# Performance work log

Hardware: AMD Instinct MI355X
Metric: run time of the kernel (lower is better)

Reference implementation:

```python
import jax, jax.numpy as jnp
import numpy as np

BS, L, D = 16, 256, 512
H, DQ, DV, DFF, KSZ = 8, 64, 64, 2048, 3


def _ln(x, g, b, eps=1e-5):
    mu = jnp.mean(x, -1, keepdims=True)
    var = jnp.mean((x - mu) ** 2, -1, keepdims=True)
    return (x - mu) / jnp.sqrt(var + eps) * g + b


def _conv(x, w):
    # x: [bs, 1, d] (NCW), w: [1, 1, k], same padding for odd k, no bias
    pad = (w.shape[-1] - 1) // 2
    return jax.lax.conv_general_dilated(x, w, (1,), [(pad, pad)], dimension_numbers=('NCH', 'OIH', 'NCH'))


def setup_inputs() -> dict:
    key = jax.random.key(0)
    ks = jax.random.split(key, 12)
    s = lambda k, shape, sc: jax.random.normal(k, shape, jnp.float32) * sc
    w0 = 0.02
    return {
        'inp': jax.random.normal(ks[0], (BS, L, D), jnp.float32),
        'conv1_w': s(ks[1], (1, 1, KSZ), 0.3),
        'conv2_w': s(ks[2], (1, 1, KSZ), 0.3),
        'ctx_wq': s(ks[3], (D, H * DQ), w0),
        'ctx_wk': s(ks[4], (D, H * DQ), w0),
        'ctx_fc': s(ks[5], (H * DV, D), w0),
        'glb_wq': s(ks[6], (D, H * DQ), w0),
        'glb_wk': s(ks[7], (D, H * DQ), w0),
        'glb_fc': s(ks[8], (H * DV, D), w0),
        'ln1_g': jnp.ones(D), 'ln1_b': jnp.zeros(D),
        'ln2_g': jnp.ones(D), 'ln2_b': jnp.zeros(D),
        'ln3_g': jnp.ones(D), 'ln3_b': jnp.zeros(D),
        'mlp_w1': s(ks[9], (D, DFF), w0), 'mlp_b1': jnp.zeros(DFF),
        'mlp_w2': s(ks[10], (DFF, D), w0), 'mlp_b2': jnp.zeros(D),
    }


def reference(inp, conv1_w, conv2_w, ctx_wq, ctx_wk, ctx_fc,
              glb_wq, glb_wk, glb_fc, ln1_g, ln1_b, ln2_g, ln2_b,
              ln3_g, ln3_b, mlp_w1, mlp_b1, mlp_w2, mlp_b2):
    bs, seqlen, d = inp.shape
    scale = 1.0 / jnp.sqrt(jnp.float32(DQ))
    # Global K/V are step-invariant: hoist out of the recurrence.
    # NOTE: original module (faithfully) projects V with W_Q, not W_V.
    Kg = (inp @ glb_wk).reshape(bs, seqlen, H, DQ).transpose(0, 2, 1, 3)  # [b,h,L,dq]
    Vg = (inp @ glb_wq).reshape(bs, seqlen, H, DV).transpose(0, 2, 1, 3)  # [b,h,L,dv]

    def step(hn, x_i):
        # hn: [bs,1,d] recurrent state, x_i: [bs,d] current token
        x = x_i[:, None, :]                                   # [bs,1,d]
        res = x
        xc = _conv(x, conv1_w)                                # [bs,1,d]
        # context cross-attn: Q=hn, K=xc, V=xc (via W_Q, as in source)
        Qc = (hn @ ctx_wq).reshape(bs, 1, H, DQ).transpose(0, 2, 1, 3)
        Kc = (xc @ ctx_wk).reshape(bs, 1, H, DQ).transpose(0, 2, 1, 3)
        Vc = (xc @ ctx_wq).reshape(bs, 1, H, DV).transpose(0, 2, 1, 3)
        sc = jnp.einsum('bhqd,bhkd->bhqk', Qc, Kc) * scale    # [b,h,1,1]
        ac = jax.nn.softmax(sc, axis=-1)
        ctx = jnp.einsum('bhqk,bhkd->bhqd', ac, Vc)
        ctx = ctx.transpose(0, 2, 1, 3).reshape(bs, 1, H * DV) @ ctx_fc
        x = _ln(ctx + res, ln1_g, ln1_b)
        res = x
        x2 = _conv(x, conv2_w)
        # global cross-attn: Q=x2, K/V from full input (hoisted)
        Qg = (x2 @ glb_wq).reshape(bs, 1, H, DQ).transpose(0, 2, 1, 3)
        sg = jnp.einsum('bhqd,bhkd->bhqk', Qg, Kg) * scale    # [b,h,1,L]
        h = jnp.einsum('bhqk,bhkd->bhqd', jax.nn.softmax(sg, axis=-1), Vg)
        h = h.transpose(0, 2, 1, 3).reshape(bs, 1, H * DV) @ glb_fc  # [bs,1,d]
        x = _ln(h + res, ln2_g, ln2_b)
        y = jax.nn.gelu(x @ mlp_w1 + mlp_b1, approximate=False) @ mlp_w2 + mlp_b2
        y = _ln(y + x, ln3_g, ln3_b)
        return h, y[:, 0, :]

    hn0 = inp[:, 0:1, :]
    hn, ys = jax.lax.scan(step, hn0, jnp.swapaxes(inp, 0, 1))  # ys: [L,bs,d]
    output = jnp.swapaxes(ys, 0, 1)                            # [bs,L,d]
    return output, hn
```

## Files before the change

kernel.cpp:

```cpp
#include <hip/hip_runtime.h>
#include <math.h>

#define NBS 16
#define NL 256
#define ND 512
#define NH 8
#define NDFF 2048
#define NT (NBS*NL)

typedef unsigned short u16;
typedef unsigned int   u32;
typedef __attribute__((ext_vector_type(8))) short bf16x8;
typedef __attribute__((ext_vector_type(4))) float f32x4;

__device__ __forceinline__ u16 f2b(float f){
  u32 u = __float_as_uint(f);
  u32 r = u + 0x7FFFu + ((u >> 16) & 1u);
  return (u16)(r >> 16);
}
__device__ __forceinline__ float blo(u32 u){ return __uint_as_float(u << 16); }
__device__ __forceinline__ float bhi(u32 u){ return __uint_as_float(u & 0xFFFF0000u); }
__device__ __forceinline__ u32 pk2(float a, float b){ return (u32)f2b(a) | ((u32)f2b(b) << 16); }

__device__ __forceinline__ void gl16(const void* g, void* l){
  __builtin_amdgcn_global_load_lds((const __attribute__((address_space(1))) void*)g,
                                   (__attribute__((address_space(3))) void*)l, 16, 0, 0);
}
__device__ __forceinline__ float gelu_f(float x){ return 0.5f*x*(1.f+erff(x*0.70710678118654752f)); }

__device__ inline void tr_tile(const float* __restrict__ src, u16* __restrict__ dst,
                               int K, int N, int ntk, int tb, float* Tsh){
  int tk = tb % ntk, tn = tb / ntk;
  int t = threadIdx.x;
  int r = t >> 2, q = t & 3;
  const float* s = src + (size_t)(tk*64 + r)*N + tn*64 + q*16;
  #pragma unroll
  for (int u2 = 0; u2 < 4; u2++){
    float4 v = *(const float4*)(s + u2*4);
    Tsh[r*65 + q*16 + u2*4 + 0] = v.x;
    Tsh[r*65 + q*16 + u2*4 + 1] = v.y;
    Tsh[r*65 + q*16 + u2*4 + 2] = v.z;
    Tsh[r*65 + q*16 + u2*4 + 3] = v.w;
  }
  __syncthreads();
  int n = t >> 2, kq = t & 3;
  u16* d = dst + (size_t)(tn*64 + n)*K + tk*64 + kq*16;
  u32 u[8];
  #pragma unroll
  for (int j = 0; j < 8; j++){
    u32 lo = f2b(Tsh[(kq*16 + 2*j    )*65 + n]);
    u32 hi = f2b(Tsh[(kq*16 + 2*j + 1)*65 + n]);
    u[j] = lo | (hi << 16);
  }
  ((uint4*)d)[0] = make_uint4(u[0],u[1],u[2],u[3]);
  ((uint4*)d)[1] = make_uint4(u[4],u[5],u[6],u[7]);
}

__global__ __launch_bounds__(256) void pack_k(
    const float* __restrict__ inp,
    const float* __restrict__ ctx_wq, const float* __restrict__ ctx_fc,
    const float* __restrict__ glb_wq, const float* __restrict__ glb_wk,
    const float* __restrict__ glb_fc,
    const float* __restrict__ w1, const float* __restrict__ w2,
    const float* __restrict__ c1w,
    u16* wk_t, u16* wq_t, u16* cfc_t, u16* gfc_t, u16* cwq_bf,
    u16* w1_t, u16* w2_t, u16* inp_bf, u16* xc_bf)
{
  __shared__ float Tsh[64*65];
  int bx = blockIdx.x, t = threadIdx.x;
  if (bx < 256){
    int m = bx >> 6, tb = bx & 63;
    const float* s; u16* d;
    if      (m == 0){ s = glb_wk; d = wk_t; }
    else if (m == 1){ s = glb_wq; d = wq_t; }
    else if (m == 2){ s = ctx_fc; d = cfc_t; }
    else            { s = glb_fc; d = gfc_t; }
    tr_tile(s, d, 512, 512, 8, tb, Tsh);
  } else if (bx < 512){
    tr_tile(w1, w1_t, 512, 2048, 8, bx - 256, Tsh);
  } else if (bx < 768){
    tr_tile(w2, w2_t, 2048, 512, 32, bx - 512, Tsh);
  } else if (bx < 1792){
    size_t i0 = (size_t)(bx - 768)*2048 + (size_t)t*8;
    float4 v0 = *(const float4*)(inp + i0);
    float4 v1 = *(const float4*)(inp + i0 + 4);
    uint4 o;
    o.x = pk2(v0.x, v0.y); o.y = pk2(v0.z, v0.w);
    o.z = pk2(v1.x, v1.y); o.w = pk2(v1.z, v1.w);
    *(uint4*)(inp_bf + i0) = o;
  } else if (bx < 2816){
    size_t i0 = (size_t)(bx - 1792)*2048 + (size_t)t*8;
    float w0 = c1w[0], w1v = c1w[1], w2v = c1w[2];
    u32 u[4];
    #pragma unroll
    for (int j = 0; j < 8; j += 2){
      float f[2];
      #pragma unroll
      for (int s2 = 0; s2 < 2; s2++){
        size_t i = i0 + j + s2; int d = (int)(i & (ND-1));
        float xm = d        ? inp[i-1] : 0.f;
        float x0 = inp[i];
        float xp = (d<ND-1) ? inp[i+1] : 0.f;
        f[s2] = w0*xm + w1v*x0 + w2v*xp;
      }
      u[j>>1] = pk2(f[0], f[1]);
    }
    *(uint4*)(xc_bf + i0) = make_uint4(u[0],u[1],u[2],u[3]);
  } else {
    size_t i0 = (size_t)(bx - 2816)*2048 + (size_t)t*8;
    float4 v0 = *(const float4*)(ctx_wq + i0);
    float4 v1 = *(const float4*)(ctx_wq + i0 + 4);
    uint4 o;
    o.x = pk2(v0.x, v0.y); o.y = pk2(v0.z, v0.w);
    o.z = pk2(v1.x, v1.y); o.w = pk2(v1.z, v1.w);
    *(uint4*)(cwq_bf + i0) = o;
  }
}

template<int BIAS,int ACT>
__device__ __forceinline__ void gemm128_core(const u16* __restrict__ A,
    const u16* __restrict__ Bt, const float* __restrict__ bias,
    void* __restrict__ Cb, int N, int K, int lda, int ldb, int outm,
    u16* sm, int row0, int col0)
{
  const int tid = threadIdx.x;
  const int w = tid >> 6, l = tid & 63;
  const int wr = w >> 1, wc = w & 1;
  const int l15 = l & 15, lk = (l >> 4)*16;
  const int srow = tid >> 3;
  const int scol = (((tid & 7)*16) ^ ((srow & 7) << 4)) >> 1;
  const u16* pa = A  + (size_t)(row0 + srow)*lda + scol;
  const u16* pb = Bt + (size_t)(col0 + srow)*ldb + scol;
  char* lA = (char*)sm + (tid & ~63)*16;
  char* lB = (char*)sm + 32768 + (tid & ~63)*16;

  f32x4 acc[4][4] = {};
  const int nt = K >> 6;

  auto STAGE = [&](int buf, int kt){
    char* a = lA + buf*16384;
    char* b = lB + buf*16384;
    #pragma unroll
    for (int i = 0; i < 4; i++){
      gl16(pa + kt + (size_t)(i*32)*lda, a + i*4096);
      gl16(pb + kt + (size_t)(i*32)*ldb, b + i*4096);
    }
  };

  STAGE(0, 0);
  __syncthreads();
  for (int t = 0; t < nt; ++t){
    if (t + 1 < nt) STAGE((t+1) & 1, (t+1)*64);
    const char* bA = (const char*)sm + (t&1)*16384;
    const char* bB = (const char*)sm + 32768 + (t&1)*16384;
    #pragma unroll
    for (int ks = 0; ks < 2; ks++){
      bf16x8 af[4], bv[4];
      #pragma unroll
      for (int m = 0; m < 4; m++){
        int r = wr*64 + m*16 + l15;
        af[m] = *(const bf16x8*)(bA + r*128 + ((ks*64 + lk) ^ ((r & 7) << 4)));
      }
      #pragma unroll
      for (int n = 0; n < 4; n++){
        int r = wc*64 + n*16 + l15;
        bv[n] = *(const bf16x8*)(bB + r*128 + ((ks*64 + lk) ^ ((r & 7) << 4)));
      }
      #pragma unroll
      for (int m = 0; m < 4; m++)
        #pragma unroll
        for (int n = 0; n < 4; n++)
          acc[m][n] = __builtin_amdgcn_mfma_f32_16x16x32_bf16(af[m], bv[n], acc[m][n], 0, 0, 0);
    }
    __syncthreads();
  }

  #pragma unroll
  for (int m = 0; m < 4; m++){
    #pragma unroll
    for (int n = 0; n < 4; n++){
      int col = col0 + wc*64 + n*16 + l15;
      int rowb = row0 + wr*64 + m*16 + (l >> 4)*4;
      if (outm == 2){
        uint2 o;
        o.x = pk2(acc[m][n][0], acc[m][n][1]);
        o.y = pk2(acc[m][n][2], acc[m][n][3]);
        *(uint2*)((u16*)Cb + (size_t)(rowb >> 8)*131072 + (size_t)col*256 + (rowb & 255)) = o;
      } else if (outm == 0){
        #pragma unroll
        for (int rr = 0; rr < 4; rr++)
          ((float*)Cb)[(size_t)(rowb + rr)*N + col] = acc[m][n][rr];
      } else {
        #pragma unroll
        for (int rr = 0; rr < 4; rr++){
          float v = acc[m][n][rr];
          if (BIAS) v += bias[col];
          if (ACT)  v = gelu_f(v);
          ((u16*)Cb)[(size_t)(rowb + rr)*N + col] = f2b(v);
        }
      }
    }
  }
}

template<int BIAS,int ACT>
__global__ __launch_bounds__(256) void gemm128_k(const u16* __restrict__ A,
                                                 const u16* __restrict__ Bt,
                                                 const float* __restrict__ bias,
                                                 void* __restrict__ Cb, int N, int K)
{
  __shared__ u16 sm[32768];
  gemm128_core<BIAS,ACT>(A, Bt, bias, Cb, N, K, K, K, 1, sm,
                         blockIdx.y*128, blockIdx.x*128);
}

__global__ __launch_bounds__(256) void gemm3_k(
    const u16* __restrict__ A0, const u16* __restrict__ B0, u16* __restrict__ C0,
    const u16* __restrict__ A1, const u16* __restrict__ B1, u16* __restrict__ C1,
    const u16* __restrict__ A2, const u16* __restrict__ B2, u16* __restrict__ C2)
{
  __shared__ u16 sm[32768];
  const u16 *A, *Bt; u16* Cb; int outm = 1;
  if (blockIdx.z == 0){ A = A0; Bt = B0; Cb = C0; }
  else if (blockIdx.z == 1){ A = A1; Bt = B1; Cb = C1; outm = 2; }
  else { A = A2; Bt = B2; Cb = C2; }
  gemm128_core<0,0>(A, Bt, nullptr, Cb, 512, 512, 512, 512, outm, sm,
                    blockIdx.y*128, blockIdx.x*128);
}

__global__ __launch_bounds__(256) void gemm_w2sk(const u16* __restrict__ G,
                                                 const u16* __restrict__ w2t,
                                                 float* __restrict__ P)
{
  __shared__ u16 sm[32768];
  const int z = blockIdx.z;
  gemm128_core<0,0>(G + z*1024, w2t + z*1024, nullptr,
                    (void*)(P + (size_t)z*NT*512), 512, 1024, 2048, 2048, 0,
                    sm, blockIdx.y*128, blockIdx.x*128);
}

__global__ __launch_bounds__(256) void gemm64_k(const u16* __restrict__ A,
                                                const u16* __restrict__ Bt,
                                                u16* __restrict__ Cb, int N, int K)
{
  __shared__ u16 sm[16384];
  const int tid = threadIdx.x;
  const int w = tid >> 6, l = tid & 63;
  const int wr = w >> 1, wc = w & 1;
  const int l15 = l & 15, lk = (l >> 4)*16;
  const int row0 = blockIdx.y*64, col0 = blockIdx.x*64;
  const int srow = tid >> 3;
  const int scol = (((tid & 7)*16) ^ ((srow & 7) << 4)) >> 1;
  const u16* pa = A  + (size_t)(row0 + srow)*K + scol;
  const u16* pb = Bt + (size_t)(col0 + srow)*K + scol;
  char* lA = (char*)sm + (tid & ~63)*16;

  f32x4 acc[2][2] = {};
  const int nt = K >> 6;
  auto STAGE = [&](int buf, int kt){
    char* a = lA + buf*8192;
    char* b = lA + 16384 + buf*8192;
    gl16(pa + kt,                a);
    gl16(pa + kt + (size_t)32*K, a + 4096);
    gl16(pb + kt,                b);
    gl16(pb + kt + (size_t)32*K, b + 4096);
  };
  STAGE(0, 0);
  __syncthreads();
  for (int t = 0; t < nt; ++t){
    if (t + 1 < nt) STAGE((t+1) & 1, (t+1)*64);
    const char* bA = (const char*)sm + (t&1)*8192;
    const char* bB = (const char*)sm + 16384 + (t&1)*8192;
    #pragma unroll
    for (int ks = 0; ks < 2; ks++){
      bf16x8 af[2], bv[2];
      #pragma unroll
      for (int m = 0; m < 2; m++){
        int r = wr*32 + m*16 + l15;
        af[m] = *(const bf16x8*)(bA + r*128 + ((ks*64 + lk) ^ ((r & 7) << 4)));
      }
      #pragma unroll
      for (int n = 0; n < 2; n++){
        int r = wc*32 + n*16 + l15;
        bv[n] = *(const bf16x8*)(bB + r*128 + ((ks*64 + lk) ^ ((r & 7) << 4)));
      }
      #pragma unroll
      for (int m = 0; m < 2; m++)
        #pragma unroll
        for (int n = 0; n < 2; n++)
          acc[m][n] = __builtin_amdgcn_mfma_f32_16x16x32_bf16(af[m], bv[n], acc[m][n], 0, 0, 0);
    }
    __syncthreads();
  }
  #pragma unroll
  for (int m = 0; m < 2; m++){
    #pragma unroll
    for (int n = 0; n < 2; n++){
      int col = col0 + wc*32 + n*16 + l15;
      int rowb = row0 + wr*32 + m*16 + (l >> 4)*4;
      #pragma unroll
      for (int rr = 0; rr < 4; rr++)
        Cb[(size_t)(rowb + rr)*N + col] = f2b(acc[m][n][rr]);
    }
  }
}

__global__ __launch_bounds__(256) void qattn_k(const u16* __restrict__ X2,
                                               const u16* __restrict__ Wq,
                                               const u16* __restrict__ Kg,
                                               const u16* __restrict__ Vt,
                                               u16* __restrict__ O)
{
  __shared__ u16 sm[40960];
  const int h = blockIdx.x, ty = blockIdx.y;
  const int b = ty >> 2, bh = b*8 + h;
  const int tid = threadIdx.x;
  const int w = tid >> 6, l = tid & 63;
  const int l15 = l & 15, lg = l >> 4;
  const int wr = w >> 1, wc = w & 1;
  const int lk = lg*16;

  {
    const int vrow = tid >> 5;
    const int vcb  = (tid*16) & 511;
    const int scolV = (vcb ^ ((vrow & 7) << 4)) >> 1;
    const u16* pv = Vt + (size_t)bh*16384 + (size_t)vrow*256 + scolV;
    char* lV = (char*)sm + 40960 + (tid & ~63)*16;
    #pragma unroll
    for (int c = 0; c < 8; c++)
      gl16(pv + (size_t)(c*8)*256, lV + c*4096);
  }

  const int srow = tid >> 3;
  const int scol = (((tid & 7)*16) ^ ((srow & 7) << 4)) >> 1;
  const u16* pa = X2 + (size_t)(ty*64 + srow)*512 + scol;
  const u16* pb = Wq + (size_t)(h*64  + srow)*512 + scol;
  char* lS = (char*)sm + (tid & ~63)*16;

  auto QSTG = [&](int buf, int kt){
    char* a = lS + buf*8192;
    char* bq = lS + 16384 + buf*8192;
    gl16(pa + kt,              a);
    gl16(pa + kt + 32*512,     a + 4096);
    gl16(pb + kt,              bq);
    gl16(pb + kt + 32*512,     bq + 4096);
  };

  f32x4 qacc[2][2] = {};
  QSTG(0, 0);
  __syncthreads();
  for (int t = 0; t < 8; ++t){
    if (t < 7) QSTG((t+1) & 1, (t+1)*64);
    const char* bA = (const char*)sm + (t&1)*8192;
    const char* bB = (const char*)sm + 16384 + (t&1)*8192;
    #pragma unroll
    for (int ks = 0; ks < 2; ks++){
      bf16x8 af[2], bv[2];
      #pragma unroll
      for (int m = 0; m < 2; m++){
        int r = wr*32 + m*16 + l15;
        af[m] = *(const bf16x8*)(bA + r*128 + ((ks*64 + lk) ^ ((r & 7) << 4)));
      }
      #pragma unroll
      for (int n = 0; n < 2; n++){
        int r = wc*32 + n*16 + l15;
        bv[n] = *(const bf16x8*)(bB + r*128 + ((ks*64 + lk) ^ ((r & 7) << 4)));
      }
      #pragma unroll
      for (int m = 0; m < 2; m++)
        #pragma unroll
        for (int n = 0; n < 2; n++)
          qacc[m][n] = __builtin_amdgcn_mfma_f32_16x16x32_bf16(af[m], bv[n], qacc[m][n], 0, 0, 0);
    }
    __syncthreads();
  }

  {
    const u16* pk = Kg + (size_t)(b*256 + srow)*512 + h*64 + scol;
    char* lK = (char*)sm + (tid & ~63)*16;
    #pragma unroll
    for (int c = 0; c < 8; c++)
      gl16(pk + (size_t)(c*32)*512, lK + c*4096);
  }
  #pragma unroll
  for (int m = 0; m < 2; m++)
    #pragma unroll
    for (int n = 0; n < 2; n++)
      #pragma unroll
      for (int rr = 0; rr < 4; rr++){
        int row = wr*32 + m*16 + (l >> 4)*4 + rr;
        int col = wc*32 + n*16 + l15;
        *(u16*)((char*)sm + 32768 + row*128 + ((col*2) ^ ((row & 7) << 4))) = f2b(qacc[m][n][rr]);
      }
  __syncthreads();

  const int qt0 = b*256 + (ty & 3)*64 + w*16;
  bf16x8 aq[2];
  #pragma unroll
  for (int ks = 0; ks < 2; ks++){
    int qr = w*16 + l15;
    aq[ks] = *(const bf16x8*)((char*)sm + 32768 + qr*128 + ((ks*64 + lk) ^ ((qr & 7) << 4)));
  }
  char* Pw = (char*)sm + 73728 + w*2048;

  f32x4 oacc[4] = {};
  float rsum[4] = {0.f, 0.f, 0.f, 0.f};

  #pragma unroll
  for (int c = 0; c < 4; c++){
    f32x4 sacc[4] = {};
    #pragma unroll
    for (int n = 0; n < 4; n++){
      int r = c*64 + n*16 + l15;
      #pragma unroll
      for (int ks = 0; ks < 2; ks++){
        bf16x8 bk = *(const bf16x8*)((const char*)sm + r*128 + ((ks*64 + lk) ^ ((r & 7) << 4)));
        sacc[n] = __builtin_amdgcn_mfma_f32_16x16x32_bf16(aq[ks], bk, sacc[n], 0, 0, 0);
      }
    }
    #pragma unroll
    for (int n = 0; n < 4; n++){
      #pragma unroll
      for (int rr = 0; rr < 4; rr++){
        float p = __expf(sacc[n][rr]*0.125f);
        rsum[rr] += p;
        int q = lg*4 + rr, key = n*16 + l15;
        *(u16*)(Pw + ((q*128 + key*2) ^ ((q & 7) << 4))) = f2b(p);
      }
    }
    bf16x8 ap[2];
    #pragma unroll
    for (int ks2 = 0; ks2 < 2; ks2++)
      ap[ks2] = *(const bf16x8*)(Pw + l15*128 + ((ks2*64 + lk) ^ ((l15 & 7) << 4)));
    #pragma unroll
    for (int n = 0; n < 4; n++){
      int r = n*16 + l15;
      #pragma unroll
      for (int ks2 = 0; ks2 < 2; ks2++){
        bf16x8 bvv = *(const bf16x8*)((const char*)sm + 40960 + r*512 +
                                      ((c*128 + ks2*64 + lk) ^ ((r & 7) << 4)));
        oacc[n] = __builtin_amdgcn_mfma_f32_16x16x32_bf16(ap[ks2], bvv, oacc[n], 0, 0, 0);
      }
    }
  }

  #pragma unroll
  for (int m = 1; m < 16; m <<= 1){
    #pragma unroll
    for (int rr = 0; rr < 4; rr++) rsum[rr] += __shfl_xor(rsum[rr], m);
  }
  #pragma unroll
  for (int n = 0; n < 4; n++){
    int d = h*64 + n*16 + l15;
    #pragma unroll
    for (int rr = 0; rr < 4; rr++){
      int t = qt0 + lg*4 + rr;
      O[(size_t)t*ND + d] = f2b(oacc[n][rr]/rsum[rr]);
    }
  }
}

template<int MODE>
__global__ __launch_bounds__(256) void ln_k(const void* __restrict__ aptr,
                                            const void* __restrict__ bptr,
                                            const float* __restrict__ g,
                                            const float* __restrict__ be,
                                            const float* __restrict__ cw,
                                            const float* __restrict__ a2,
                                            const float* __restrict__ bias2,
                                            u16* __restrict__ obf,
                                            u16* __restrict__ convbf,
                                            float* __restrict__ of32,
                                            float* __restrict__ hnout)
{
  __shared__ float row[512];
  __shared__ float red[10];
  const int r0 = blockIdx.x, tid = threadIdx.x;
  const size_t base = (size_t)r0*ND;
  const int d = tid*2;
  float v0, v1;
  if (MODE == 3){
    float2 p0 = *(const float2*)((const float*)aptr + base + d);
    float2 p1 = *(const float2*)(a2 + base + d);
    u32 bv = *(const u32*)((const u16*)bptr + base + d);
    v0 = p0.x + p1.x + bias2[d]   + blo(bv);
    v1 = p0.y + p1.y + bias2[d+1] + bhi(bv);
  } else {
    u32 av = *(const u32*)((const u16*)aptr + base + d);
    v0 = blo(av); v1 = bhi(av);
    if (MODE == 1 && (r0 & 255) == 255){
      hnout[(size_t)(r0 >> 8)*512 + d]     = v0;
      hnout[(size_t)(r0 >> 8)*512 + d + 1] = v1;
    }
    if (MODE == 0){
      float2 bv = *(const float2*)((const float*)bptr + base + d);
      v0 += bv.x; v1 += bv.y;
    } else {
      u32 bv = *(const u32*)((const u16*)bptr + base + d);
      v0 += blo(bv); v1 += bhi(bv);
    }
  }
  float s = v0+v1, ss = v0*v0+v1*v1;
  #pragma unroll
  for (int m = 1; m < 64; m <<= 1){ s += __shfl_xor(s, m); ss += __shfl_xor(ss, m); }
  int wv = tid >> 6;
  if ((tid & 63) == 0){ red[wv] = s; red[4+wv] = ss; }
  __syncthreads();
  if (tid == 0){
    float S = red[0]+red[1]+red[2]+red[3];
    float SS = red[4]+red[5]+red[6]+red[7];
    float mu = S*(1.f/ND);
    float var = SS*(1.f/ND) - mu*mu;
    red[8] = mu; red[9] = rsqrtf(var + 1e-5f);
  }
  __syncthreads();
  float mu = red[8], rsd = red[9];
  float o0 = (v0-mu)*rsd*g[d]   + be[d];
  float o1 = (v1-mu)*rsd*g[d+1] + be[d+1];
  if (MODE == 3){
    *(float2*)(of32 + base + d) = make_float2(o0, o1);
  } else {
    *(u32*)(obf + base + d) = pk2(o0, o1);
    if (MODE == 0){
      row[d] = o0; row[d+1] = o1;
      __syncthreads();
      float w0 = cw[0], w1v = cw[1], w2v = cw[2];
      float xm = d ? row[d-1] : 0.f;
      float xp2 = (d+2 < 512) ? row[d+2] : 0.f;
      float c0 = w0*xm + w1v*o0 + w2v*o1;
      float c1 = w0*o0 + w1v*o1 + w2v*xp2;
      *(u32*)(convbf + base + d) = pk2(c0, c1);
    }
  }
}

extern "C" void kernel_launch(void* const* d_in, const int* in_sizes, int n_in,
                              void* d_out, int out_size, void* d_ws, size_t ws_size,
                              hipStream_t stream) {
  const float* inp     = (const float*)d_in[0];
  const float* conv1_w = (const float*)d_in[1];
  const float* conv2_w = (const float*)d_in[2];
  const float* ctx_wq  = (const float*)d_in[3];
  const float* ctx_fc  = (const float*)d_in[5];
  const float* glb_wq  = (const float*)d_in[6];
  const float* glb_wk  = (const float*)d_in[7];
  const float* glb_fc  = (const float*)d_in[8];
  const float* ln1_g = (const float*)d_in[9],  *ln1_b = (const float*)d_in[10];
  const float* ln2_g = (const float*)d_in[11], *ln2_b = (const float*)d_in[12];
  const float* ln3_g = (const float*)d_in[13], *ln3_b = (const float*)d_in[14];
  const float* mlp_w1 = (const float*)d_in[15], *mlp_b1 = (const float*)d_in[16];
  const float* mlp_w2 = (const float*)d_in[17], *mlp_b2 = (const float*)d_in[18];
  float* out = (float*)d_out;
  float* hn  = out + (size_t)NT*ND;

  u16* wk_t   = (u16*)d_ws;
  u16* wq_t   = wk_t   + 262144;
  u16* cfc_t  = wq_t   + 262144;
  u16* gfc_t  = cfc_t  + 262144;
  u16* cwq_bf = gfc_t  + 262144;
  u16* Wc_t   = cwq_bf + 262144;
  u16* w1_t   = Wc_t   + 262144;
  u16* w2_t   = w1_t   + 1048576;
  u16* inp_bf = w2_t   + 1048576;
  u16* Abf    = inp_bf + 2097152;
  u16* Bbf    = Abf    + 2097152;
  u16* Cbf    = Bbf    + 2097152;
  u16* Kg     = Cbf    + 2097152;
  u16* Vt     = Kg     + 2097152;
  u16* X1bf   = Vt     + 2097152;
  u16* X3bf   = X1bf   + 2097152;
  u16* Gbf    = X3bf   + 2097152;
  float* Pf   = (float*)(Gbf + 8388608);

  pack_k<<<2944, 256, 0, stream>>>(inp, ctx_wq, ctx_fc, glb_wq, glb_wk, glb_fc,
                                   mlp_w1, mlp_w2, conv1_w,
                                   wk_t, wq_t, cfc_t, gfc_t, cwq_bf, w1_t, w2_t,
                                   inp_bf, Abf);
  gemm64_k<<<dim3(8,8),256,0,stream>>>(cfc_t, cwq_bf, Wc_t, 512, 512);
  gemm3_k<<<dim3(4,32,3),256,0,stream>>>(inp_bf, wk_t, Kg,
                                         inp_bf, wq_t, Vt,
                                         Abf,    Wc_t, Cbf);
  ln_k<0><<<NT,256,0,stream>>>(Cbf, inp, ln1_g, ln1_b, conv2_w, nullptr, nullptr,
                               X1bf, Abf, nullptr, nullptr);
  qattn_k<<<dim3(8,64),256,0,stream>>>(Abf, wq_t, Kg, Vt, Bbf);
  gemm64_k<<<dim3(8,64),256,0,stream>>>(Bbf, gfc_t, Cbf, 512, 512);
  ln_k<1><<<NT,256,0,stream>>>(Cbf, X1bf, ln2_g, ln2_b, nullptr, nullptr, nullptr,
                               X3bf, nullptr, nullptr, hn);
  gemm128_k<1,1><<<dim3(16,32),256,0,stream>>>(X3bf, w1_t, mlp_b1, Gbf, 2048, 512);
  gemm_w2sk<<<dim3(4,32,2),256,0,stream>>>(Gbf, w2_t, Pf);
  ln_k<3><<<NT,256,0,stream>>>(Pf, X3bf, ln3_g, ln3_b, nullptr, Pf + (size_t)NT*512,
                               mlp_b2, nullptr, nullptr, out, nullptr);
}
```

Baseline: 104.3 us.

## Shrink GEMM tiles and drop LDS double-buffering for higher occupancy

Replaces the 128x128 double-buffered GEMM core and the separate 64x64 kernel with one templated core using TMx64 tiles (TM=64 or 128) and a single LDS buffer, synchronised before and after each K-tile load. Launch grids are enlarged to match: more blocks for the QKV, MLP-up and MLP-down GEMMs, and smaller LDS and register footprints per block. The aim is more blocks and waves per CU on these mid-sized GEMMs. The cost is losing the load/compute overlap from double buffering and getting less data reuse per tile.

```diff
diff --git a/kernel.cpp b/kernel.cpp
--- a/kernel.cpp
+++ b/kernel.cpp
@@ -117,12 +117,13 @@
   }
 }
 
-template<int BIAS,int ACT>
-__device__ __forceinline__ void gemm128_core(const u16* __restrict__ A,
+template<int TM,int BIAS,int ACT>
+__device__ __forceinline__ void gemm2p_core(const u16* __restrict__ A,
     const u16* __restrict__ Bt, const float* __restrict__ bias,
     void* __restrict__ Cb, int N, int K, int lda, int ldb, int outm,
     u16* sm, int row0, int col0)
 {
+  constexpr int MF = TM/32;
   const int tid = threadIdx.x;
   const int w = tid >> 6, l = tid & 63;
   const int wr = w >> 1, wc = w & 1;
@@ -132,55 +133,48 @@
   const u16* pa = A  + (size_t)(row0 + srow)*lda + scol;
   const u16* pb = Bt + (size_t)(col0 + srow)*ldb + scol;
   char* lA = (char*)sm + (tid & ~63)*16;
-  char* lB = (char*)sm + 32768 + (tid & ~63)*16;
-
-  f32x4 acc[4][4] = {};
+  char* lB = (char*)sm + TM*128 + (tid & ~63)*16;
+
+  f32x4 acc[MF][2] = {};
   const int nt = K >> 6;
 
-  auto STAGE = [&](int buf, int kt){
-    char* a = lA + buf*16384;
-    char* b = lB + buf*16384;
-    #pragma unroll
-    for (int i = 0; i < 4; i++){
-      gl16(pa + kt + (size_t)(i*32)*lda, a + i*4096);
-      gl16(pb + kt + (size_t)(i*32)*ldb, b + i*4096);
-    }
-  };
-
-  STAGE(0, 0);
-  __syncthreads();
   for (int t = 0; t < nt; ++t){
-    if (t + 1 < nt) STAGE((t+1) & 1, (t+1)*64);
-    const char* bA = (const char*)sm + (t&1)*16384;
-    const char* bB = (const char*)sm + 32768 + (t&1)*16384;
+    __syncthreads();
+    #pragma unroll
+    for (int i = 0; i < MF; i++)
+      gl16(pa + t*64 + (size_t)(i*32)*lda, lA + i*4096);
+    gl16(pb + t*64,                  lB);
+    gl16(pb + t*64 + (size_t)32*ldb, lB + 4096);
+    __syncthreads();
+    const char* bA = (const char*)sm;
+    const char* bB = (const char*)sm + TM*128;
     #pragma unroll
     for (int ks = 0; ks < 2; ks++){
-      bf16x8 af[4], bv[4];
-      #pragma unroll
-      for (int m = 0; m < 4; m++){
-        int r = wr*64 + m*16 + l15;
+      bf16x8 af[MF], bv[2];
+      #pragma unroll
+      for (int m = 0; m < MF; m++){
+        int r = wr*(TM/2) + m*16 + l15;
         af[m] = *(const bf16x8*)(bA + r*128 + ((ks*64 + lk) ^ ((r & 7) << 4)));
       }
       #pragma unroll
-      for (int n = 0; n < 4; n++){
-        int r = wc*64 + n*16 + l15;
+      for (int n = 0; n < 2; n++){
+        int r = wc*32 + n*16 + l15;
         bv[n] = *(const bf16x8*)(bB + r*128 + ((ks*64 + lk) ^ ((r & 7) << 4)));
       }
       #pragma unroll
-      for (int m = 0; m < 4; m++)
+      for (int m = 0; m < MF; m++)
         #pragma unroll
-        for (int n = 0; n < 4; n++)
+        for (int n = 0; n < 2; n++)
           acc[m][n] = __builtin_amdgcn_mfma_f32_16x16x32_bf16(af[m], bv[n], acc[m][n], 0, 0, 0);
     }
-    __syncthreads();
-  }
-
-  #pragma unroll
-  for (int m = 0; m < 4; m++){
-    #pragma unroll
-    for (int n = 0; n < 4; n++){
-      int col = col0 + wc*64 + n*16 + l15;
-      int rowb = row0 + wr*64 + m*16 + (l >> 4)*4;
+  }
+
+  #pragma unroll
+  for (int m = 0; m < MF; m++){
+    #pragma unroll
+    for (int n = 0; n < 2; n++){
+      int col = col0 + wc*32 + n*16 + l15;
+      int rowb = row0 + wr*(TM/2) + m*16 + (l >> 4)*4;
       if (outm == 2){
         uint2 o;
         o.x = pk2(acc[m][n][0], acc[m][n][1]);
@@ -203,15 +197,15 @@
   }
 }
 
-template<int BIAS,int ACT>
-__global__ __launch_bounds__(256) void gemm128_k(const u16* __restrict__ A,
-                                                 const u16* __restrict__ Bt,
-                                                 const float* __restrict__ bias,
-                                                 void* __restrict__ Cb, int N, int K)
-{
-  __shared__ u16 sm[32768];
-  gemm128_core<BIAS,ACT>(A, Bt, bias, Cb, N, K, K, K, 1, sm,
-                         blockIdx.y*128, blockIdx.x*128);
+template<int TM,int BIAS,int ACT>
+__global__ __launch_bounds__(256) void gemm_k(const u16* __restrict__ A,
+                                              const u16* __restrict__ Bt,
+                                              const float* __restrict__ bias,
+                                              void* __restrict__ Cb, int N, int K)
+{
+  __shared__ u16 sm[TM*64 + 4096];
+  gemm2p_core<TM,BIAS,ACT>(A, Bt, bias, Cb, N, K, K, K, 1, sm,
+                           blockIdx.y*TM, blockIdx.x*64);
 }
 
 __global__ __launch_bounds__(256) void gemm3_k(
@@ -219,90 +213,24 @@
     const u16* __restrict__ A1, const u16* __restrict__ B1, u16* __restrict__ C1,
     const u16* __restrict__ A2, const u16* __restrict__ B2, u16* __restrict__ C2)
 {
-  __shared__ u16 sm[32768];
+  __shared__ u16 sm[128*64 + 4096];
   const u16 *A, *Bt; u16* Cb; int outm = 1;
   if (blockIdx.z == 0){ A = A0; Bt = B0; Cb = C0; }
   else if (blockIdx.z == 1){ A = A1; Bt = B1; Cb = C1; outm = 2; }
   else { A = A2; Bt = B2; Cb = C2; }
-  gemm128_core<0,0>(A, Bt, nullptr, Cb, 512, 512, 512, 512, outm, sm,
-                    blockIdx.y*128, blockIdx.x*128);
+  gemm2p_core<128,0,0>(A, Bt, nullptr, Cb, 512, 512, 512, 512, outm, sm,
+                       blockIdx.y*128, blockIdx.x*64);
 }
 
 __global__ __launch_bounds__(256) void gemm_w2sk(const u16* __restrict__ G,
                                                  const u16* __restrict__ w2t,
                                                  float* __restrict__ P)
 {
-  __shared__ u16 sm[32768];
+  __shared__ u16 sm[64*64 + 4096];
   const int z = blockIdx.z;
-  gemm128_core<0,0>(G + z*1024, w2t + z*1024, nullptr,
-                    (void*)(P + (size_t)z*NT*512), 512, 1024, 2048, 2048, 0,
-                    sm, blockIdx.y*128, blockIdx.x*128);
-}
-
-__global__ __launch_bounds__(256) void gemm64_k(const u16* __restrict__ A,
-                                                const u16* __restrict__ Bt,
-                                                u16* __restrict__ Cb, int N, int K)
-{
-  __shared__ u16 sm[16384];
-  const int tid = threadIdx.x;
-  const int w = tid >> 6, l = tid & 63;
-  const int wr = w >> 1, wc = w & 1;
-  const int l15 = l & 15, lk = (l >> 4)*16;
-  const int row0 = blockIdx.y*64, col0 = blockIdx.x*64;
-  const int srow = tid >> 3;
-  const int scol = (((tid & 7)*16) ^ ((srow & 7) << 4)) >> 1;
-  const u16* pa = A  + (size_t)(row0 + srow)*K + scol;
-  const u16* pb = Bt + (size_t)(col0 + srow)*K + scol;
-  char* lA = (char*)sm + (tid & ~63)*16;
-
-  f32x4 acc[2][2] = {};
-  const int nt = K >> 6;
-  auto STAGE = [&](int buf, int kt){
-    char* a = lA + buf*8192;
-    char* b = lA + 16384 + buf*8192;
-    gl16(pa + kt,                a);
-    gl16(pa + kt + (size_t)32*K, a + 4096);
-    gl16(pb + kt,                b);
-    gl16(pb + kt + (size_t)32*K, b + 4096);
-  };
-  STAGE(0, 0);
-  __syncthreads();
-  for (int t = 0; t < nt; ++t){
-    if (t + 1 < nt) STAGE((t+1) & 1, (t+1)*64);
-    const char* bA = (const char*)sm + (t&1)*8192;
-    const char* bB = (const char*)sm + 16384 + (t&1)*8192;
-    #pragma unroll
-    for (int ks = 0; ks < 2; ks++){
-      bf16x8 af[2], bv[2];
-      #pragma unroll
-      for (int m = 0; m < 2; m++){
-        int r = wr*32 + m*16 + l15;
-        af[m] = *(const bf16x8*)(bA + r*128 + ((ks*64 + lk) ^ ((r & 7) << 4)));
-      }
-      #pragma unroll
-      for (int n = 0; n < 2; n++){
-        int r = wc*32 + n*16 + l15;
-        bv[n] = *(const bf16x8*)(bB + r*128 + ((ks*64 + lk) ^ ((r & 7) << 4)));
-      }
-      #pragma unroll
-      for (int m = 0; m < 2; m++)
-        #pragma unroll
-        for (int n = 0; n < 2; n++)
-          acc[m][n] = __builtin_amdgcn_mfma_f32_16x16x32_bf16(af[m], bv[n], acc[m][n], 0, 0, 0);
-    }
-    __syncthreads();
-  }
-  #pragma unroll
-  for (int m = 0; m < 2; m++){
-    #pragma unroll
-    for (int n = 0; n < 2; n++){
-      int col = col0 + wc*32 + n*16 + l15;
-      int rowb = row0 + wr*32 + m*16 + (l >> 4)*4;
-      #pragma unroll
-      for (int rr = 0; rr < 4; rr++)
-        Cb[(size_t)(rowb + rr)*N + col] = f2b(acc[m][n][rr]);
-    }
-  }
+  gemm2p_core<64,0,0>(G + z*1024, w2t + z*1024, nullptr,
+                      (void*)(P + (size_t)z*NT*512), 512, 1024, 2048, 2048, 0,
+                      sm, blockIdx.y*64, blockIdx.x*64);
 }
 
 __global__ __launch_bounds__(256) void qattn_k(const u16* __restrict__ X2,
@@ -576,18 +504,18 @@
                                    mlp_w1, mlp_w2, conv1_w,
                                    wk_t, wq_t, cfc_t, gfc_t, cwq_bf, w1_t, w2_t,
                                    inp_bf, Abf);
-  gemm64_k<<<dim3(8,8),256,0,stream>>>(cfc_t, cwq_bf, Wc_t, 512, 512);
-  gemm3_k<<<dim3(4,32,3),256,0,stream>>>(inp_bf, wk_t, Kg,
+  gemm_k<64,0,0><<<dim3(8,8),256,0,stream>>>(cfc_t, cwq_bf, nullptr, Wc_t, 512, 512);
+  gemm3_k<<<dim3(8,32,3),256,0,stream>>>(inp_bf, wk_t, Kg,
                                          inp_bf, wq_t, Vt,
                                          Abf,    Wc_t, Cbf);
   ln_k<0><<<NT,256,0,stream>>>(Cbf, inp, ln1_g, ln1_b, conv2_w, nullptr, nullptr,
                                X1bf, Abf, nullptr, nullptr);
   qattn_k<<<dim3(8,64),256,0,stream>>>(Abf, wq_t, Kg, Vt, Bbf);
-  gemm64_k<<<dim3(8,64),256,0,stream>>>(Bbf, gfc_t, Cbf, 512, 512);
+  gemm_k<64,0,0><<<dim3(8,64),256,0,stream>>>(Bbf, gfc_t, nullptr, Cbf, 512, 512);
   ln_k<1><<<NT,256,0,stream>>>(Cbf, X1bf, ln2_g, ln2_b, nullptr, nullptr, nullptr,
                                X3bf, nullptr, nullptr, hn);
-  gemm128_k<1,1><<<dim3(16,32),256,0,stream>>>(X3bf, w1_t, mlp_b1, Gbf, 2048, 512);
-  gemm_w2sk<<<dim3(4,32,2),256,0,stream>>>(Gbf, w2_t, Pf);
+  gemm_k<128,1,1><<<dim3(32,32),256,0,stream>>>(X3bf, w1_t, mlp_b1, Gbf, 2048, 512);
+  gemm_w2sk<<<dim3(8,64,2),256,0,stream>>>(Gbf, w2_t, Pf);
   ln_k<3><<<NT,256,0,stream>>>(Pf, X3bf, ln3_g, ln3_b, nullptr, Pf + (size_t)NT*512,
                                mlp_b2, nullptr, nullptr, out, nullptr);
 }
```

New measurement: 113.7 us. 9.1% more time.

## Use fine-grained waitcnt barriers in GEMM loops and 4-way bf16 split-K for W2

Applied to the files above, without the earlier changes.

The GEMM main loops replace the __syncthreads pairs with an explicit s_waitcnt on outstanding global-to-LDS loads plus a raw s_barrier. This lets the next stage's prefetch stay in flight while the current tile is consumed. The MLP down-projection now uses a 4-way split-K with bf16 partial outputs instead of a 2-way split with fp32 partials, which adds parallelism and halves partial-sum traffic. The cost is lower precision in the partial sums. The conv pack step also reuses vector loads instead of issuing scalar neighbour loads.

```diff
diff --git a/kernel.cpp b/kernel.cpp
--- a/kernel.cpp
+++ b/kernel.cpp
@@ -90,21 +90,18 @@
     *(uint4*)(inp_bf + i0) = o;
   } else if (bx < 2816){
     size_t i0 = (size_t)(bx - 1792)*2048 + (size_t)t*8;
+    int d0 = (int)(i0 & (ND-1));
     float w0 = c1w[0], w1v = c1w[1], w2v = c1w[2];
+    float4 v0 = *(const float4*)(inp + i0);
+    float4 v1 = *(const float4*)(inp + i0 + 4);
+    float xm = (d0 > 0)      ? inp[i0 - 1] : 0.f;
+    float xp = (d0 < ND - 8) ? inp[i0 + 8] : 0.f;
+    float x[10] = {xm, v0.x,v0.y,v0.z,v0.w, v1.x,v1.y,v1.z,v1.w, xp};
     u32 u[4];
     #pragma unroll
-    for (int j = 0; j < 8; j += 2){
-      float f[2];
-      #pragma unroll
-      for (int s2 = 0; s2 < 2; s2++){
-        size_t i = i0 + j + s2; int d = (int)(i & (ND-1));
-        float xm = d        ? inp[i-1] : 0.f;
-        float x0 = inp[i];
-        float xp = (d<ND-1) ? inp[i+1] : 0.f;
-        f[s2] = w0*xm + w1v*x0 + w2v*xp;
-      }
-      u[j>>1] = pk2(f[0], f[1]);
-    }
+    for (int j = 0; j < 8; j += 2)
+      u[j>>1] = pk2(w0*x[j] + w1v*x[j+1] + w2v*x[j+2],
+                    w0*x[j+1] + w1v*x[j+2] + w2v*x[j+3]);
     *(uint4*)(xc_bf + i0) = make_uint4(u[0],u[1],u[2],u[3]);
   } else {
     size_t i0 = (size_t)(bx - 2816)*2048 + (size_t)t*8;
@@ -148,9 +145,15 @@
   };
 
   STAGE(0, 0);
-  __syncthreads();
   for (int t = 0; t < nt; ++t){
-    if (t + 1 < nt) STAGE((t+1) & 1, (t+1)*64);
+    if (t + 1 < nt){
+      STAGE((t+1) & 1, (t+1)*64);
+      asm volatile("s_waitcnt vmcnt(8)" ::: "memory");
+    } else {
+      asm volatile("s_waitcnt vmcnt(0)" ::: "memory");
+    }
+    __builtin_amdgcn_s_barrier();
+    __builtin_amdgcn_sched_barrier(0);
     const char* bA = (const char*)sm + (t&1)*16384;
     const char* bB = (const char*)sm + 32768 + (t&1)*16384;
     #pragma unroll
@@ -172,7 +175,8 @@
         for (int n = 0; n < 4; n++)
           acc[m][n] = __builtin_amdgcn_mfma_f32_16x16x32_bf16(af[m], bv[n], acc[m][n], 0, 0, 0);
     }
-    __syncthreads();
+    asm volatile("s_waitcnt lgkmcnt(0)" ::: "memory");
+    __builtin_amdgcn_s_barrier();
   }
 
   #pragma unroll
@@ -230,12 +234,12 @@
 
 __global__ __launch_bounds__(256) void gemm_w2sk(const u16* __restrict__ G,
                                                  const u16* __restrict__ w2t,
-                                                 float* __restrict__ P)
+                                                 u16* __restrict__ P4)
 {
   __shared__ u16 sm[32768];
   const int z = blockIdx.z;
-  gemm128_core<0,0>(G + z*1024, w2t + z*1024, nullptr,
-                    (void*)(P + (size_t)z*NT*512), 512, 1024, 2048, 2048, 0,
+  gemm128_core<0,0>(G + z*512, w2t + z*512, nullptr,
+                    (void*)(P4 + (size_t)z*NT*512), 512, 512, 2048, 2048, 1,
                     sm, blockIdx.y*128, blockIdx.x*128);
 }
 
@@ -266,9 +270,15 @@
     gl16(pb + kt + (size_t)32*K, b + 4096);
   };
   STAGE(0, 0);
-  __syncthreads();
   for (int t = 0; t < nt; ++t){
-    if (t + 1 < nt) STAGE((t+1) & 1, (t+1)*64);
+    if (t + 1 < nt){
+      STAGE((t+1) & 1, (t+1)*64);
+      asm volatile("s_waitcnt vmcnt(4)" ::: "memory");
+    } else {
+      asm volatile("s_waitcnt vmcnt(0)" ::: "memory");
+    }
+    __builtin_amdgcn_s_barrier();
+    __builtin_amdgcn_sched_barrier(0);
     const char* bA = (const char*)sm + (t&1)*8192;
     const char* bB = (const char*)sm + 16384 + (t&1)*8192;
     #pragma unroll
@@ -290,7 +300,8 @@
         for (int n = 0; n < 2; n++)
           acc[m][n] = __builtin_amdgcn_mfma_f32_16x16x32_bf16(af[m], bv[n], acc[m][n], 0, 0, 0);
     }
-    __syncthreads();
+    asm volatile("s_waitcnt lgkmcnt(0)" ::: "memory");
+    __builtin_amdgcn_s_barrier();
   }
   #pragma unroll
   for (int m = 0; m < 2; m++){
@@ -466,7 +477,6 @@
                                             const float* __restrict__ g,
                                             const float* __restrict__ be,
                                             const float* __restrict__ cw,
-                                            const float* __restrict__ a2,
                                             const float* __restrict__ bias2,
                                             u16* __restrict__ obf,
                                             u16* __restrict__ convbf,
@@ -480,11 +490,14 @@
   const int d = tid*2;
   float v0, v1;
   if (MODE == 3){
-    float2 p0 = *(const float2*)((const float*)aptr + base + d);
-    float2 p1 = *(const float2*)(a2 + base + d);
+    const u16* p4 = (const u16*)aptr;
+    u32 q0 = *(const u32*)(p4 + base + d);
+    u32 q1 = *(const u32*)(p4 + 2097152 + base + d);
+    u32 q2 = *(const u32*)(p4 + 4194304 + base + d);
+    u32 q3 = *(const u32*)(p4 + 6291456 + base + d);
     u32 bv = *(const u32*)((const u16*)bptr + base + d);
-    v0 = p0.x + p1.x + bias2[d]   + blo(bv);
-    v1 = p0.y + p1.y + bias2[d+1] + bhi(bv);
+    v0 = blo(q0)+blo(q1)+blo(q2)+blo(q3) + bias2[d]   + blo(bv);
+    v1 = bhi(q0)+bhi(q1)+bhi(q2)+bhi(q3) + bias2[d+1] + bhi(bv);
   } else {
     u32 av = *(const u32*)((const u16*)aptr + base + d);
     v0 = blo(av); v1 = bhi(av);
@@ -570,7 +583,7 @@
   u16* X1bf   = Vt     + 2097152;
   u16* X3bf   = X1bf   + 2097152;
   u16* Gbf    = X3bf   + 2097152;
-  float* Pf   = (float*)(Gbf + 8388608);
+  u16* P4     = Gbf    + 8388608;
 
   pack_k<<<2944, 256, 0, stream>>>(inp, ctx_wq, ctx_fc, glb_wq, glb_wk, glb_fc,
                                    mlp_w1, mlp_w2, conv1_w,
@@ -580,14 +593,14 @@
   gemm3_k<<<dim3(4,32,3),256,0,stream>>>(inp_bf, wk_t, Kg,
                                          inp_bf, wq_t, Vt,
                                          Abf,    Wc_t, Cbf);
-  ln_k<0><<<NT,256,0,stream>>>(Cbf, inp, ln1_g, ln1_b, conv2_w, nullptr, nullptr,
+  ln_k<0><<<NT,256,0,stream>>>(Cbf, inp, ln1_g, ln1_b, conv2_w, nullptr,
                                X1bf, Abf, nullptr, nullptr);
   qattn_k<<<dim3(8,64),256,0,stream>>>(Abf, wq_t, Kg, Vt, Bbf);
   gemm64_k<<<dim3(8,64),256,0,stream>>>(Bbf, gfc_t, Cbf, 512, 512);
-  ln_k<1><<<NT,256,0,stream>>>(Cbf, X1bf, ln2_g, ln2_b, nullptr, nullptr, nullptr,
+  ln_k<1><<<NT,256,0,stream>>>(Cbf, X1bf, ln2_g, ln2_b, nullptr, nullptr,
                                X3bf, nullptr, nullptr, hn);
   gemm128_k<1,1><<<dim3(16,32),256,0,stream>>>(X3bf, w1_t, mlp_b1, Gbf, 2048, 512);
-  gemm_w2sk<<<dim3(4,32,2),256,0,stream>>>(Gbf, w2_t, Pf);
-  ln_k<3><<<NT,256,0,stream>>>(Pf, X3bf, ln3_g, ln3_b, nullptr, Pf + (size_t)NT*512,
+  gemm_w2sk<<<dim3(4,32,4),256,0,stream>>>(Gbf, w2_t, P4);
+  ln_k<3><<<NT,256,0,stream>>>(P4, X3bf, ln3_g, ln3_b, nullptr,
                                mlp_b2, nullptr, nullptr, out, nullptr);
 }
```

Result: slower. 112.3 us (+7.7%).

## Fold conv1d weights into projection matrices and compute combined ctx weight in pack kernel

Applied to the files above, without the earlier changes.

The 3-tap convolutions are linear along the feature dimension, so they are folded into the weights instead of being applied to activations. conv2 is baked into a transposed copy of glb_wq used by the query-attention kernel. conv1 is folded into the fused ctx_wq·ctx_fc matrix, which is now built by an fp32 FMA tile loop inside pack_k. This removes the separate gemm64 launch, the conv-on-input pass, and the conv branch in the first layernorm, and lets gemm3 share one A operand, cutting launches and activation traffic. In exchange, pack_k does a small scalar fp32 GEMM, and the attention queries see bf16-rounded folded weights, so rounding differs slightly from before.

```diff
diff --git a/kernel.cpp b/kernel.cpp
--- a/kernel.cpp
+++ b/kernel.cpp
@@ -56,26 +56,64 @@
   ((uint4*)d)[1] = make_uint4(u[4],u[5],u[6],u[7]);
 }
 
+__device__ inline void tr_tile_conv(const float* __restrict__ src, u16* __restrict__ dst,
+                                    int tb, const float* __restrict__ cw, float* Tsh){
+  int tk = tb & 7, tn = tb >> 3;
+  int t = threadIdx.x;
+  int r = t >> 2, q = t & 3;
+  const float* s = src + (size_t)(tk*64 + r)*512 + tn*64 + q*16;
+  #pragma unroll
+  for (int u2 = 0; u2 < 4; u2++){
+    float4 v = *(const float4*)(s + u2*4);
+    Tsh[(r+1)*65 + q*16 + u2*4 + 0] = v.x;
+    Tsh[(r+1)*65 + q*16 + u2*4 + 1] = v.y;
+    Tsh[(r+1)*65 + q*16 + u2*4 + 2] = v.z;
+    Tsh[(r+1)*65 + q*16 + u2*4 + 3] = v.w;
+  }
+  if (t < 64){
+    Tsh[t] = (tk > 0) ? src[(size_t)(tk*64 - 1)*512 + tn*64 + t] : 0.f;
+  } else if (t < 128){
+    int tt = t - 64;
+    Tsh[65*65 + tt] = (tk < 7) ? src[(size_t)(tk*64 + 64)*512 + tn*64 + tt] : 0.f;
+  }
+  __syncthreads();
+  float c0 = cw[0], c1 = cw[1], c2 = cw[2];
+  int n = t >> 2, kq = t & 3;
+  u16* d = dst + (size_t)(tn*64 + n)*512 + tk*64 + kq*16;
+  u32 u[8];
+  #pragma unroll
+  for (int j = 0; j < 8; j++){
+    float lo = c0*Tsh[(kq*16 + 2*j + 2)*65 + n] + c1*Tsh[(kq*16 + 2*j + 1)*65 + n]
+             + c2*Tsh[(kq*16 + 2*j    )*65 + n];
+    float hi = c0*Tsh[(kq*16 + 2*j + 3)*65 + n] + c1*Tsh[(kq*16 + 2*j + 2)*65 + n]
+             + c2*Tsh[(kq*16 + 2*j + 1)*65 + n];
+    u[j] = pk2(lo, hi);
+  }
+  ((uint4*)d)[0] = make_uint4(u[0],u[1],u[2],u[3]);
+  ((uint4*)d)[1] = make_uint4(u[4],u[5],u[6],u[7]);
+}
+
 __global__ __launch_bounds__(256) void pack_k(
     const float* __restrict__ inp,
     const float* __restrict__ ctx_wq, const float* __restrict__ ctx_fc,
     const float* __restrict__ glb_wq, const float* __restrict__ glb_wk,
     const float* __restrict__ glb_fc,
     const float* __restrict__ w1, const float* __restrict__ w2,
-    const float* __restrict__ c1w,
-    u16* wk_t, u16* wq_t, u16* cfc_t, u16* gfc_t, u16* cwq_bf,
-    u16* w1_t, u16* w2_t, u16* inp_bf, u16* xc_bf)
-{
-  __shared__ float Tsh[64*65];
+    const float* __restrict__ c1w, const float* __restrict__ c2w,
+    u16* wk_t, u16* wq_t, u16* wq2_t, u16* gfc_t, u16* Wc_t,
+    u16* w1_t, u16* w2_t, u16* inp_bf)
+{
+  __shared__ float Tsh[66*65];
   int bx = blockIdx.x, t = threadIdx.x;
-  if (bx < 256){
+  if (bx < 192){
     int m = bx >> 6, tb = bx & 63;
     const float* s; u16* d;
     if      (m == 0){ s = glb_wk; d = wk_t; }
     else if (m == 1){ s = glb_wq; d = wq_t; }
-    else if (m == 2){ s = ctx_fc; d = cfc_t; }
     else            { s = glb_fc; d = gfc_t; }
     tr_tile(s, d, 512, 512, 8, tb, Tsh);
+  } else if (bx < 256){
+    tr_tile_conv(glb_wq, wq2_t, bx - 192, c2w, Tsh);
   } else if (bx < 512){
     tr_tile(w1, w1_t, 512, 2048, 8, bx - 256, Tsh);
   } else if (bx < 768){
@@ -88,32 +126,49 @@
     o.x = pk2(v0.x, v0.y); o.y = pk2(v0.z, v0.w);
     o.z = pk2(v1.x, v1.y); o.w = pk2(v1.z, v1.w);
     *(uint4*)(inp_bf + i0) = o;
-  } else if (bx < 2816){
-    size_t i0 = (size_t)(bx - 1792)*2048 + (size_t)t*8;
-    float w0 = c1w[0], w1v = c1w[1], w2v = c1w[2];
-    u32 u[4];
-    #pragma unroll
-    for (int j = 0; j < 8; j += 2){
-      float f[2];
-      #pragma unroll
-      for (int s2 = 0; s2 < 2; s2++){
-        size_t i = i0 + j + s2; int d = (int)(i & (ND-1));
-        float xm = d        ? inp[i-1] : 0.f;
-        float x0 = inp[i];
-        float xp = (d<ND-1) ? inp[i+1] : 0.f;
-        f[s2] = w0*xm + w1v*x0 + w2v*xp;
-      }
-      u[j>>1] = pk2(f[0], f[1]);
-    }
-    *(uint4*)(xc_bf + i0) = make_uint4(u[0],u[1],u[2],u[3]);
   } else {
-    size_t i0 = (size_t)(bx - 2816)*2048 + (size_t)t*8;
-    float4 v0 = *(const float4*)(ctx_wq + i0);
-    float4 v1 = *(const float4*)(ctx_wq + i0 + 4);
-    uint4 o;
-    o.x = pk2(v0.x, v0.y); o.y = pk2(v0.z, v0.w);
-    o.z = pk2(v1.x, v1.y); o.w = pk2(v1.z, v1.w);
-    *(uint4*)(cwq_bf + i0) = o;
+    float* Fsh = Tsh;
+    float* Qsh = Tsh + 2048;
+    int tb = bx - 1792;
+    int n0 = (tb >> 3)*64, e0 = (tb & 7)*64;
+    float c0 = c1w[0], c1 = c1w[1], c2 = c1w[2];
+    int tr = t >> 4, tc = t & 15;
+    float acc[4][4] = {};
+    for (int mc = 0; mc < 32; mc++){
+      int m0 = mc*16;
+      __syncthreads();
+      #pragma unroll
+      for (int i = 0; i < 4; i++){
+        int idx = t + i*256;
+        int fr = idx >> 6, fc = idx & 63;
+        Fsh[fr*65 + fc] = ctx_fc[(size_t)(m0 + fr)*512 + n0 + fc];
+        int qe = idx >> 4, qm = idx & 15;
+        int ge = e0 + qe;
+        float a  = ctx_wq[(size_t)ge*512 + m0 + qm];
+        float bm = (ge > 0)   ? ctx_wq[(size_t)(ge-1)*512 + m0 + qm] : 0.f;
+        float cp = (ge < 511) ? ctx_wq[(size_t)(ge+1)*512 + m0 + qm] : 0.f;
+        Qsh[qe*17 + qm] = c0*cp + c1*a + c2*bm;
+      }
+      __syncthreads();
+      #pragma unroll
+      for (int m = 0; m < 16; m++){
+        float fv[4], qv[4];
+        #pragma unroll
+        for (int j = 0; j < 4; j++) fv[j] = Fsh[m*65 + tc*4 + j];
+        #pragma unroll
+        for (int i = 0; i < 4; i++) qv[i] = Qsh[(tr*4 + i)*17 + m];
+        #pragma unroll
+        for (int i = 0; i < 4; i++)
+          #pragma unroll
+          for (int j = 0; j < 4; j++)
+            acc[i][j] += qv[i]*fv[j];
+      }
+    }
+    #pragma unroll
+    for (int i = 0; i < 4; i++)
+      #pragma unroll
+      for (int j = 0; j < 4; j++)
+        Wc_t[(size_t)(n0 + tc*4 + j)*512 + e0 + tr*4 + i] = f2b(acc[i][j]);
   }
 }
 
@@ -215,15 +270,16 @@
 }
 
 __global__ __launch_bounds__(256) void gemm3_k(
-    const u16* __restrict__ A0, const u16* __restrict__ B0, u16* __restrict__ C0,
-    const u16* __restrict__ A1, const u16* __restrict__ B1, u16* __restrict__ C1,
-    const u16* __restrict__ A2, const u16* __restrict__ B2, u16* __restrict__ C2)
+    const u16* __restrict__ A,
+    const u16* __restrict__ B0, u16* __restrict__ C0,
+    const u16* __restrict__ B1, u16* __restrict__ C1,
+    const u16* __restrict__ B2, u16* __restrict__ C2)
 {
   __shared__ u16 sm[32768];
-  const u16 *A, *Bt; u16* Cb; int outm = 1;
-  if (blockIdx.z == 0){ A = A0; Bt = B0; Cb = C0; }
-  else if (blockIdx.z == 1){ A = A1; Bt = B1; Cb = C1; outm = 2; }
-  else { A = A2; Bt = B2; Cb = C2; }
+  const u16 *Bt; u16* Cb; int outm = 1;
+  if (blockIdx.z == 0){ Bt = B0; Cb = C0; }
+  else if (blockIdx.z == 1){ Bt = B1; Cb = C1; outm = 2; }
+  else { Bt = B2; Cb = C2; }
   gemm128_core<0,0>(A, Bt, nullptr, Cb, 512, 512, 512, 512, outm, sm,
                     blockIdx.y*128, blockIdx.x*128);
 }
@@ -305,8 +361,8 @@
   }
 }
 
-__global__ __launch_bounds__(256) void qattn_k(const u16* __restrict__ X2,
-                                               const u16* __restrict__ Wq,
+__global__ __launch_bounds__(256) void qattn_k(const u16* __restrict__ X1,
+                                               const u16* __restrict__ Wq2,
                                                const u16* __restrict__ Kg,
                                                const u16* __restrict__ Vt,
                                                u16* __restrict__ O)
@@ -333,8 +389,8 @@
 
   const int srow = tid >> 3;
   const int scol = (((tid & 7)*16) ^ ((srow & 7) << 4)) >> 1;
-  const u16* pa = X2 + (size_t)(ty*64 + srow)*512 + scol;
-  const u16* pb = Wq + (size_t)(h*64  + srow)*512 + scol;
+  const u16* pa = X1 + (size_t)(ty*64 + srow)*512 + scol;
+  const u16* pb = Wq2 + (size_t)(h*64 + srow)*512 + scol;
   char* lS = (char*)sm + (tid & ~63)*16;
 
   auto QSTG = [&](int buf, int kt){
@@ -465,15 +521,12 @@
                                             const void* __restrict__ bptr,
                                             const float* __restrict__ g,
                                             const float* __restrict__ be,
-                                            const float* __restrict__ cw,
                                             const float* __restrict__ a2,
                                             const float* __restrict__ bias2,
                                             u16* __restrict__ obf,
-                                            u16* __restrict__ convbf,
                                             float* __restrict__ of32,
                                             float* __restrict__ hnout)
 {
-  __shared__ float row[512];
   __shared__ float red[10];
   const int r0 = blockIdx.x, tid = threadIdx.x;
   const size_t base = (size_t)r0*ND;
@@ -521,16 +574,6 @@
     *(float2*)(of32 + base + d) = make_float2(o0, o1);
   } else {
     *(u32*)(obf + base + d) = pk2(o0, o1);
-    if (MODE == 0){
-      row[d] = o0; row[d+1] = o1;
-      __syncthreads();
-      float w0 = cw[0], w1v = cw[1], w2v = cw[2];
-      float xm = d ? row[d-1] : 0.f;
-      float xp2 = (d+2 < 512) ? row[d+2] : 0.f;
-      float c0 = w0*xm + w1v*o0 + w2v*o1;
-      float c1 = w0*o0 + w1v*o1 + w2v*xp2;
-      *(u32*)(convbf + base + d) = pk2(c0, c1);
-    }
   }
 }
 
@@ -555,16 +598,14 @@
 
   u16* wk_t   = (u16*)d_ws;
   u16* wq_t   = wk_t   + 262144;
-  u16* cfc_t  = wq_t   + 262144;
-  u16* gfc_t  = cfc_t  + 262144;
-  u16* cwq_bf = gfc_t  + 262144;
-  u16* Wc_t   = cwq_bf + 262144;
+  u16* wq2_t  = wq_t   + 262144;
+  u16* gfc_t  = wq2_t  + 262144;
+  u16* Wc_t   = gfc_t  + 262144;
   u16* w1_t   = Wc_t   + 262144;
   u16* w2_t   = w1_t   + 1048576;
   u16* inp_bf = w2_t   + 1048576;
   u16* Abf    = inp_bf + 2097152;
-  u16* Bbf    = Abf    + 2097152;
-  u16* Cbf    = Bbf    + 2097152;
+  u16* Cbf    = Abf    + 2097152;
   u16* Kg     = Cbf    + 2097152;
   u16* Vt     = Kg     + 2097152;
   u16* X1bf   = Vt     + 2097152;
@@ -572,22 +613,19 @@
   u16* Gbf    = X3bf   + 2097152;
   float* Pf   = (float*)(Gbf + 8388608);
 
-  pack_k<<<2944, 256, 0, stream>>>(inp, ctx_wq, ctx_fc, glb_wq, glb_wk, glb_fc,
-                                   mlp_w1, mlp_w2, conv1_w,
-                                   wk_t, wq_t, cfc_t, gfc_t, cwq_bf, w1_t, w2_t,
-                                   inp_bf, Abf);
-  gemm64_k<<<dim3(8,8),256,0,stream>>>(cfc_t, cwq_bf, Wc_t, 512, 512);
-  gemm3_k<<<dim3(4,32,3),256,0,stream>>>(inp_bf, wk_t, Kg,
-                                         inp_bf, wq_t, Vt,
-                                         Abf,    Wc_t, Cbf);
-  ln_k<0><<<NT,256,0,stream>>>(Cbf, inp, ln1_g, ln1_b, conv2_w, nullptr, nullptr,
-                               X1bf, Abf, nullptr, nullptr);
-  qattn_k<<<dim3(8,64),256,0,stream>>>(Abf, wq_t, Kg, Vt, Bbf);
-  gemm64_k<<<dim3(8,64),256,0,stream>>>(Bbf, gfc_t, Cbf, 512, 512);
-  ln_k<1><<<NT,256,0,stream>>>(Cbf, X1bf, ln2_g, ln2_b, nullptr, nullptr, nullptr,
-                               X3bf, nullptr, nullptr, hn);
+  pack_k<<<1856, 256, 0, stream>>>(inp, ctx_wq, ctx_fc, glb_wq, glb_wk, glb_fc,
+                                   mlp_w1, mlp_w2, conv1_w, conv2_w,
+                                   wk_t, wq_t, wq2_t, gfc_t, Wc_t, w1_t, w2_t,
+                                   inp_bf);
+  gemm3_k<<<dim3(4,32,3),256,0,stream>>>(inp_bf, wk_t, Kg, wq_t, Vt, Wc_t, Cbf);
+  ln_k<0><<<NT,256,0,stream>>>(Cbf, inp, ln1_g, ln1_b, nullptr, nullptr,
+                               X1bf, nullptr, nullptr);
+  qattn_k<<<dim3(8,64),256,0,stream>>>(X1bf, wq2_t, Kg, Vt, Abf);
+  gemm64_k<<<dim3(8,64),256,0,stream>>>(Abf, gfc_t, Cbf, 512, 512);
+  ln_k<1><<<NT,256,0,stream>>>(Cbf, X1bf, ln2_g, ln2_b, nullptr, nullptr,
+                               X3bf, nullptr, hn);
   gemm128_k<1,1><<<dim3(16,32),256,0,stream>>>(X3bf, w1_t, mlp_b1, Gbf, 2048, 512);
   gemm_w2sk<<<dim3(4,32,2),256,0,stream>>>(Gbf, w2_t, Pf);
-  ln_k<3><<<NT,256,0,stream>>>(Pf, X3bf, ln3_g, ln3_b, nullptr, Pf + (size_t)NT*512,
-                               mlp_b2, nullptr, nullptr, out, nullptr);
-}
+  ln_k<3><<<NT,256,0,stream>>>(Pf, X3bf, ln3_g, ln3_b, Pf + (size_t)NT*512,
+                               mlp_b2, nullptr, out, nullptr);
+}
```

After: 172.2 us. +65.2%, slower.
